# Kernel optimization log

Measured on AMD Instinct MI355X. Metric: run time of the kernel, lower is better.

Reference implementation:

```python
import jax, jax.numpy as jnp
import numpy as np

IMAGE_SIZE = 1024      # config.model.image_size
DOWNSIZING = 64        # PromptGetter grid cell size (in upsampled pixels)
THRESHOLD = 0.65       # default_threshold_target
NUM_BG = 1             # num_bg_points
EPS = 1e-12


def setup_inputs() -> dict:
    key = jax.random.key(0)
    k1, k2 = jax.random.split(key)
    image_embeddings = jax.random.normal(k1, (1, 256, 64, 64), dtype=jnp.float32)
    reference_feats = jax.random.normal(k2, (32, 1, 256), dtype=jnp.float32)
    return {"image_embeddings": image_embeddings, "reference_feats": reference_feats}


def _point_selection(sim_up):
    """sim_up: [S, S] similarity map at original resolution.
    Returns (points_scores [n_cells, 3] as (x, y, score) sorted by score desc,
             bg_coords [NUM_BG, 2] as (x, y)).
    Faithful static-shape version of PromptGetter._point_selection: the torch
    code picks, within every DOWNSIZING x DOWNSIZING grid cell, the highest-sim
    pixel above threshold; cells with no pixel above threshold yield -1 rows."""
    n = IMAGE_SIZE // DOWNSIZING  # 16 -> 256 grid cells
    # background point: global minimum of the similarity map
    flat = sim_up.reshape(-1)
    _, bg_idx = jax.lax.top_k(-flat, NUM_BG)
    bg_row = bg_idx // IMAGE_SIZE
    bg_col = bg_idx % IMAGE_SIZE
    bg_coords = jnp.stack([bg_col, bg_row], axis=-1).astype(jnp.float32)  # (x, y)

    # foreground: per-grid-cell argmax
    cells = sim_up.reshape(n, DOWNSIZING, n, DOWNSIZING)
    cells = cells.transpose(0, 2, 1, 3).reshape(n * n, DOWNSIZING * DOWNSIZING)
    local_idx = jnp.argmax(cells, axis=-1)                                   # [n*n]
    score = jnp.take_along_axis(cells, local_idx[:, None], axis=-1)[:, 0]    # [n*n]
    cell_ids = jnp.arange(n * n)
    cy, cx = cell_ids // n, cell_ids % n
    ly, lx = local_idx // DOWNSIZING, local_idx % DOWNSIZING
    y = (cy * DOWNSIZING + ly).astype(jnp.float32)
    x = (cx * DOWNSIZING + lx).astype(jnp.float32)
    pts = jnp.stack([x, y, score], axis=-1)                                   # [n*n, 3]
    valid = score > THRESHOLD
    pts = jnp.where(valid[:, None], pts, jnp.float32(-1.0))
    order = jnp.argsort(-pts[:, 2])  # sort by score, descending; -1 rows sink
    return pts[order], bg_coords


def reference(image_embeddings, reference_feats):
    # image_embeddings: [1, C, h, w]; reference_feats: [L, 1, C]
    feat = image_embeddings[0]                                   # [C, h, w]
    C, h, w = feat.shape
    feat = feat / (jnp.linalg.norm(feat, axis=0, keepdims=True) + EPS)
    feat = feat.reshape(C, h * w)                                # [C, h*w]
    ref = reference_feats[:, 0, :]                               # [L, C]
    ref = ref / (jnp.linalg.norm(ref, axis=-1, keepdims=True) + EPS)
    sim = (ref @ feat).reshape(-1, h, w)                         # [L, h, w] cosine sim
    # postprocess_masks with original_size == image_size: one bilinear upsample
    sim_up = jax.image.resize(sim, (sim.shape[0], IMAGE_SIZE, IMAGE_SIZE), method="bilinear")
    total_points_scores, total_bg_coords = jax.vmap(_point_selection)(sim_up)
    return total_points_scores, total_bg_coords
```

## Files before the change

kernel.cpp:

```cpp
#include <hip/hip_runtime.h>
#include <math.h>

#define THRESH 0.65f


__global__ __launch_bounds__(256) void k_sim(const float* __restrict__ feat,
                                             const float* __restrict__ ref,
                                             float* __restrict__ sim) {
    __shared__ float rn0[256], rn1[256], red[256];
    __shared__ float pd0[256], pd1[256], pn[256];
    int t = threadIdx.x;
    int m0 = blockIdx.y * 2;

    float v0 = ref[m0 * 256 + t];
    float v1 = ref[(m0 + 1) * 256 + t];
    red[t] = v0 * v0;
    __syncthreads();
    for (int s = 128; s > 0; s >>= 1) { if (t < s) red[t] += red[t + s]; __syncthreads(); }
    float den0 = sqrtf(red[0]) + 1e-12f;
    __syncthreads();
    red[t] = v1 * v1;
    __syncthreads();
    for (int s = 128; s > 0; s >>= 1) { if (t < s) red[t] += red[t + s]; __syncthreads(); }
    float den1 = sqrtf(red[0]) + 1e-12f;
    rn0[t] = v0 / den0;
    rn1[t] = v1 / den1;
    __syncthreads();

    int half = t >> 7, pxl = t & 127;
    int px = blockIdx.x * 128 + pxl;
    const float* fp = feat + px + half * 128 * 4096;
    const float* r0 = rn0 + half * 128;
    const float* r1 = rn1 + half * 128;
    float d0 = 0.f, d1 = 0.f, nq = 0.f;
    for (int g = 0; g < 8; ++g) {
#pragma unroll
        for (int cc = 0; cc < 16; ++cc) {
            int c = g * 16 + cc;
            float fv = fp[c * 4096];
            d0 += fv * r0[c];
            d1 += fv * r1[c];
            nq += fv * fv;
        }
    }
    pd0[t] = d0; pd1[t] = d1; pn[t] = nq;
    __syncthreads();
    float D0 = pd0[pxl] + pd0[pxl + 128];
    float D1 = pd1[pxl] + pd1[pxl + 128];
    float NQ = pn[pxl] + pn[pxl + 128];
    float den = sqrtf(NQ) + 1e-12f;
    sim[(m0 + half) * 4096 + px] = (half ? D1 : D0) / den;
}

__global__ __launch_bounds__(256) void k_scan_out(const float* __restrict__ sim,
                                                  float* __restrict__ out) {
    __shared__ float S[64 * 65];
    __shared__ float sc[256];
    __shared__ float wmin[4];
    __shared__ int wmini[4];

    int m = blockIdx.x, t = threadIdx.x;
    const float* sm = sim + m * 4096;
    for (int k = 0; k < 16; ++k) {
        int f = t + 256 * k;
        S[(f >> 6) * 65 + (f & 63)] = sm[f];
    }
    __syncthreads();

    int cy = t >> 4, cx = t & 15;
    int gxs[6];
#pragma unroll
    for (int j = 0; j < 6; ++j) {
        int g = 4 * cx - 1 + j;
        gxs[j] = min(max(g, 0), 63);
    }
    const int   L0[5]  = {0, 8, 24, 40, 56};
    const int   L1[5]  = {7, 23, 39, 55, 63};
    const float WXA[5] = {0.53125f, 0.03125f, 0.03125f, 0.03125f, 0.03125f};
    const float WXB[5] = {0.96875f, 0.96875f, 0.96875f, 0.96875f, 0.46875f};
    const float WCA[5] = {0.46875f, 0.96875f, 0.96875f, 0.96875f, 0.96875f};
    const float WCB[5] = {0.03125f, 0.03125f, 0.03125f, 0.03125f, 0.53125f};

    float bmax = -1e30f, bmin = 1e30f;
    int bmaxi = 0, bmini = 0;
#pragma unroll
    for (int sy = 0; sy < 5; ++sy) {
#pragma unroll
        for (int e = 0; e < 2; ++e) {
            int r = e ? L1[sy] : L0[sy];
            int oy = cy * 64 + r;
            float fy = (oy + 0.5f) * 0.0625f - 0.5f;
            float y0f = floorf(fy);
            float wy = fy - y0f, w1y = 1.0f - wy;
            bool ylo = fy < 0.0f, yhi = fy > 63.0f;
            int y0 = (int)y0f;
            const float* P0 = S + min(max(y0, 0), 63) * 65;
            const float* P1 = S + min(max(y0 + 1, 0), 63) * 65;
            float q[6];
#pragma unroll
            for (int j = 0; j < 6; ++j) {
                float a = P0[gxs[j]], c = P1[gxs[j]];
                q[j] = ylo ? a : (yhi ? c : w1y * a + wy * c);
            }
#pragma unroll
            for (int s5 = 0; s5 < 5; ++s5) {
                float q0 = q[s5], q1 = q[s5 + 1];
                float va, vb;
                if (cx == 0 && s5 == 0)       { va = q1; vb = q1; }
                else if (cx == 15 && s5 == 4) { va = q0; vb = q0; }
                else {
                    va = WCA[s5] * q0 + WXA[s5] * q1;
                    vb = WCB[s5] * q0 + WXB[s5] * q1;
                }
                float smax, smin; int smaxl, sminl;
                if (va >= vb) { smax = va; smaxl = L0[s5]; } else { smax = vb; smaxl = L1[s5]; }
                if (va <= vb) { smin = va; sminl = L0[s5]; } else { smin = vb; sminl = L1[s5]; }
                if (smax > bmax) { bmax = smax; bmaxi = r * 64 + smaxl; }
                if (smin < bmin) { bmin = smin; bmini = oy * 1024 + cx * 64 + sminl; }
            }
        }
    }

    bool valid = bmax > THRESH;
    float px = valid ? (float)(cx * 64 + (bmaxi & 63)) : -1.0f;
    float py = valid ? (float)(cy * 64 + (bmaxi >> 6)) : -1.0f;
    float ps = valid ? bmax : -1.0f;
    sc[t] = ps;
    __syncthreads();
    int rank = 0;
    for (int j = 0; j < 256; ++j) {
        float sj = sc[j];
        rank += (sj > ps || (sj == ps && j < t)) ? 1 : 0;
    }
    float* o = out + m * 768 + rank * 3;
    o[0] = px; o[1] = py; o[2] = ps;

    for (int off = 32; off > 0; off >>= 1) {
        float mv = __shfl_down(bmin, off);
        int   mj = __shfl_down(bmini, off);
        if (mv < bmin || (mv == bmin && mj < bmini)) { bmin = mv; bmini = mj; }
    }
    if ((t & 63) == 0) { wmin[t >> 6] = bmin; wmini[t >> 6] = bmini; }
    __syncthreads();
    if (t == 0) {
        float bv = wmin[0]; int bi = wmini[0];
        for (int w = 1; w < 4; ++w) {
            if (wmin[w] < bv || (wmin[w] == bv && wmini[w] < bi)) {
                bv = wmin[w]; bi = wmini[w];
            }
        }
        out[24576 + m * 2 + 0] = (float)(bi % 1024);
        out[24576 + m * 2 + 1] = (float)(bi / 1024);
    }
}

extern "C" void kernel_launch(void* const* d_in, const int* in_sizes, int n_in,
                              void* d_out, int out_size, void* d_ws, size_t ws_size,
                              hipStream_t stream) {
    const float* feat = (const float*)d_in[0];
    const float* ref  = (const float*)d_in[1];
    if (in_sizes[0] == 32 * 256) {
        feat = (const float*)d_in[1];
        ref  = (const float*)d_in[0];
    }
    float* out = (float*)d_out;
    float* sim = (float*)d_ws;

    k_sim<<<dim3(32, 16), 256, 0, stream>>>(feat, ref, sim);
    k_scan_out<<<32, 256, 0, stream>>>(sim, out);
}
```

Baseline: 74.24 us.

## Vectorize similarity and scan kernels with float4 loads and wave-shuffle reductions

The sim kernel now has each thread load float4 feature vectors over a 32-channel slice, then reduces the 8 slices through shared memory. The two serial tree reductions over the reference norms become one parallel pair of wave-shuffle reductions. The scan kernel loads the sim map with float4 and reads the rank-sort scores four at a time from LDS. The aim is fewer memory instructions and fewer barriers. In exchange, the final reduction in the sim kernel runs on only 32 threads per block.

New measurement: 75.39 us. No clear change (+1.5%).

```diff
diff --git a/kernel.cpp b/kernel.cpp
--- a/kernel.cpp
+++ b/kernel.cpp
@@ -3,67 +3,84 @@
 
 #define THRESH 0.65f
 
+typedef float f4 __attribute__((ext_vector_type(4)));
+
 
 __global__ __launch_bounds__(256) void k_sim(const float* __restrict__ feat,
                                              const float* __restrict__ ref,
                                              float* __restrict__ sim) {
-    __shared__ float rn0[256], rn1[256], red[256];
-    __shared__ float pd0[256], pd1[256], pn[256];
+    __shared__ float rn0[256], rn1[256];
+    __shared__ float red0[256], red1[256];
+    __shared__ float den01[2];
+    __shared__ __align__(16) f4 pd0[256], pd1[256], pn[256];
     int t = threadIdx.x;
     int m0 = blockIdx.y * 2;
 
     float v0 = ref[m0 * 256 + t];
     float v1 = ref[(m0 + 1) * 256 + t];
-    red[t] = v0 * v0;
+    red0[t] = v0 * v0;
+    red1[t] = v1 * v1;
     __syncthreads();
-    for (int s = 128; s > 0; s >>= 1) { if (t < s) red[t] += red[t + s]; __syncthreads(); }
-    float den0 = sqrtf(red[0]) + 1e-12f;
+    int wid = t >> 6, lane = t & 63;
+    if (wid < 2) {
+        const float* src = wid ? red1 : red0;
+        float s = src[lane] + src[lane + 64] + src[lane + 128] + src[lane + 192];
+        for (int off = 32; off > 0; off >>= 1) s += __shfl_down(s, off);
+        if (lane == 0) den01[wid] = sqrtf(s) + 1e-12f;
+    }
     __syncthreads();
-    red[t] = v1 * v1;
-    __syncthreads();
-    for (int s = 128; s > 0; s >>= 1) { if (t < s) red[t] += red[t + s]; __syncthreads(); }
-    float den1 = sqrtf(red[0]) + 1e-12f;
-    rn0[t] = v0 / den0;
-    rn1[t] = v1 / den1;
+    rn0[t] = v0 / den01[0];
+    rn1[t] = v1 / den01[1];
     __syncthreads();
 
-    int half = t >> 7, pxl = t & 127;
-    int px = blockIdx.x * 128 + pxl;
-    const float* fp = feat + px + half * 128 * 4096;
-    const float* r0 = rn0 + half * 128;
-    const float* r1 = rn1 + half * 128;
-    float d0 = 0.f, d1 = 0.f, nq = 0.f;
-    for (int g = 0; g < 8; ++g) {
+    int cslice = t >> 5, q = t & 31;
+    const f4* fp4 = (const f4*)feat + blockIdx.x * 32 + q;
+    const float* r0 = rn0 + cslice * 32;
+    const float* r1 = rn1 + cslice * 32;
+    f4 d0 = 0.f, d1 = 0.f, nq = 0.f;
 #pragma unroll
-        for (int cc = 0; cc < 16; ++cc) {
-            int c = g * 16 + cc;
-            float fv = fp[c * 4096];
-            d0 += fv * r0[c];
-            d1 += fv * r1[c];
-            nq += fv * fv;
-        }
+    for (int i = 0; i < 32; ++i) {
+        f4 fv = fp4[(cslice * 32 + i) * 1024];
+        d0 += fv * r0[i];
+        d1 += fv * r1[i];
+        nq += fv * fv;
     }
     pd0[t] = d0; pd1[t] = d1; pn[t] = nq;
     __syncthreads();
-    float D0 = pd0[pxl] + pd0[pxl + 128];
-    float D1 = pd1[pxl] + pd1[pxl + 128];
-    float NQ = pn[pxl] + pn[pxl + 128];
-    float den = sqrtf(NQ) + 1e-12f;
-    sim[(m0 + half) * 4096 + px] = (half ? D1 : D0) / den;
+    if (t < 32) {
+        f4 D0 = pd0[t], D1 = pd1[t], NQ = pn[t];
+#pragma unroll
+        for (int s = 1; s < 8; ++s) {
+            D0 += pd0[s * 32 + t];
+            D1 += pd1[s * 32 + t];
+            NQ += pn[s * 32 + t];
+        }
+        f4 dn;
+        dn.x = sqrtf(NQ.x) + 1e-12f;
+        dn.y = sqrtf(NQ.y) + 1e-12f;
+        dn.z = sqrtf(NQ.z) + 1e-12f;
+        dn.w = sqrtf(NQ.w) + 1e-12f;
+        f4* so = (f4*)sim;
+        so[m0 * 1024 + blockIdx.x * 32 + t] = D0 / dn;
+        so[(m0 + 1) * 1024 + blockIdx.x * 32 + t] = D1 / dn;
+    }
 }
 
 __global__ __launch_bounds__(256) void k_scan_out(const float* __restrict__ sim,
                                                   float* __restrict__ out) {
     __shared__ float S[64 * 65];
-    __shared__ float sc[256];
+    __shared__ __align__(16) float sc[256];
     __shared__ float wmin[4];
     __shared__ int wmini[4];
 
     int m = blockIdx.x, t = threadIdx.x;
-    const float* sm = sim + m * 4096;
-    for (int k = 0; k < 16; ++k) {
-        int f = t + 256 * k;
-        S[(f >> 6) * 65 + (f & 63)] = sm[f];
+    const f4* sm4 = (const f4*)(sim + m * 4096);
+#pragma unroll
+    for (int k = 0; k < 4; ++k) {
+        int fi = k * 256 + t;
+        f4 v = sm4[fi];
+        float* dst = S + (fi >> 4) * 65 + (fi & 15) * 4;
+        dst[0] = v.x; dst[1] = v.y; dst[2] = v.z; dst[3] = v.w;
     }
     __syncthreads();
 
@@ -96,15 +113,15 @@
             int y0 = (int)y0f;
             const float* P0 = S + min(max(y0, 0), 63) * 65;
             const float* P1 = S + min(max(y0 + 1, 0), 63) * 65;
-            float q[6];
+            float qv[6];
 #pragma unroll
             for (int j = 0; j < 6; ++j) {
                 float a = P0[gxs[j]], c = P1[gxs[j]];
-                q[j] = ylo ? a : (yhi ? c : w1y * a + wy * c);
+                qv[j] = ylo ? a : (yhi ? c : w1y * a + wy * c);
             }
 #pragma unroll
             for (int s5 = 0; s5 < 5; ++s5) {
-                float q0 = q[s5], q1 = q[s5 + 1];
+                float q0 = qv[s5], q1 = qv[s5 + 1];
                 float va, vb;
                 if (cx == 0 && s5 == 0)       { va = q1; vb = q1; }
                 else if (cx == 15 && s5 == 4) { va = q0; vb = q0; }
@@ -128,9 +145,15 @@
     sc[t] = ps;
     __syncthreads();
     int rank = 0;
-    for (int j = 0; j < 256; ++j) {
-        float sj = sc[j];
-        rank += (sj > ps || (sj == ps && j < t)) ? 1 : 0;
+    const f4* sc4 = (const f4*)sc;
+#pragma unroll 8
+    for (int j4 = 0; j4 < 64; ++j4) {
+        f4 s4 = sc4[j4];
+        int j = j4 * 4;
+        rank += (s4.x > ps || (s4.x == ps && (j + 0) < t)) ? 1 : 0;
+        rank += (s4.y > ps || (s4.y == ps && (j + 1) < t)) ? 1 : 0;
+        rank += (s4.z > ps || (s4.z == ps && (j + 2) < t)) ? 1 : 0;
+        rank += (s4.w > ps || (s4.w == ps && (j + 3) < t)) ? 1 : 0;
     }
     float* o = out + m * 768 + rank * 3;
     o[0] = px; o[1] = py; o[2] = ps;
```
